# Kernel optimization log

Hardware: AMD Instinct MI355X
Metric: run time of the kernel (lower is better)

Reference implementation:

```python
import jax, jax.numpy as jnp
import numpy as np

N = 64          # num_atoms
K = 2           # num_edge_types
VDIM = 32
EDIM = 32
HID = 64        # hard-coded n_hid in the module
B = 128         # num_sims
E = N * (N - 1)
_off = ~np.eye(N, dtype=bool)
SEND, RECV = [np.asarray(a) for a in np.where(_off)]  # edge e: node SEND[e] -> node RECV[e] (NRI: rel_send=rows, rel_rec=cols)
EPS = 1e-5  # torch BatchNorm1d default


def _mlp(x, W1, b1, W2, b2, gamma, beta):
    # NRI MLP: fc1 -> ELU -> fc2 -> ELU -> BatchNorm1d (training-mode batch stats over all but last dim)
    h = jax.nn.elu(x @ W1 + b1)
    o = jax.nn.elu(h @ W2 + b2)
    ax = tuple(range(o.ndim - 1))
    mu = o.mean(ax, keepdims=True)
    var = o.var(ax, keepdims=True)  # biased variance, as torch BN uses for normalization
    return gamma * (o - mu) * jax.lax.rsqrt(var + EPS) + beta


def setup_inputs():
    key = jax.random.key(0)
    ks = jax.random.split(key, 16)
    p = lambda k, shape: jax.random.normal(k, shape, jnp.float32) * 0.05
    return {
        "v0": jax.random.normal(ks[0], (B, N, VDIM), jnp.float32),
        "e0": jax.random.normal(ks[1], (B, N, N - 1, EDIM), jnp.float32),
        "edge_type": jax.random.uniform(ks[2], (B, E, K), dtype=jnp.float32),
        "mlpv_W1": p(ks[3], (EDIM, HID)), "mlpv_b1": p(ks[4], (HID,)),
        "mlpv_W2": p(ks[5], (HID, VDIM)), "mlpv_b2": p(ks[6], (VDIM,)),
        "mlpv_gamma": jnp.ones((VDIM,), jnp.float32), "mlpv_beta": jnp.zeros((VDIM,), jnp.float32),
        "mlpe_W1": p(ks[7], (K, 2 * VDIM, HID)), "mlpe_b1": p(ks[8], (K, HID)),
        "mlpe_W2": p(ks[9], (K, HID, EDIM)), "mlpe_b2": p(ks[10], (K, EDIM)),
        "mlpe_gamma": jnp.ones((K, EDIM), jnp.float32), "mlpe_beta": jnp.zeros((K, EDIM), jnp.float32),
    }


def reference(v0, e0, edge_type, mlpv_W1, mlpv_b1, mlpv_W2, mlpv_b2, mlpv_gamma, mlpv_beta,
              mlpe_W1, mlpe_b1, mlpe_W2, mlpe_b2, mlpe_gamma, mlpe_beta):
    e0f = e0.reshape(B, E, EDIM)
    # edge2node: rel_rec.T @ e0f is exactly a scatter-add of edge states onto receiver nodes, / num_atoms
    agg = jnp.zeros((B, N, EDIM), e0f.dtype).at[:, RECV].add(e0f) / N
    dv = _mlp(agg, mlpv_W1, mlpv_b1, mlpv_W2, mlpv_b2, mlpv_gamma, mlpv_beta)  # [B,N,VDIM]
    # node2edge: rel_rec@v0 / rel_send@v0 are gathers of node states per edge
    edges = jnp.concatenate([v0[:, RECV], v0[:, SEND]], axis=-1)  # [B,E,2V]
    # all K per-edge-type MLPs in one batched einsum (replaces the Python loop)
    h = jax.nn.elu(jnp.einsum('bef,kfh->bkeh', edges, mlpe_W1) + mlpe_b1[None, :, None, :])
    o = jax.nn.elu(jnp.einsum('bkeh,kho->bkeo', h, mlpe_W2) + mlpe_b2[None, :, None, :])
    mu = o.mean((0, 2), keepdims=True)   # BN stats per edge type, over (batch, edges)
    var = o.var((0, 2), keepdims=True)
    o = mlpe_gamma[None, :, None, :] * (o - mu) * jax.lax.rsqrt(var + EPS) + mlpe_beta[None, :, None, :]
    # mask each type's message by its edge_type weight, then sum over types
    de = (o * edge_type.transpose(0, 2, 1)[..., None]).sum(1)  # [B,E,EDIM]
    de = de.reshape(B, N, N - 1, EDIM)
    return (dv, de, edge_type * 0)
```

## Files before the change

### kernel.cpp

```cpp
#include <hip/hip_runtime.h>
#include <hip/hip_bf16.h>

#define NB 128
#define NA 64
#define NE 4032
#define KT 2
#define BE (NB * NE)
#define DV_SIZE 262144
#define DE_SIZE 16515072
#define ZERO_SIZE 1032192

#define PBLK_A 1008
#define TPW_A 8

typedef __attribute__((ext_vector_type(8))) short short8;
typedef __attribute__((ext_vector_type(4))) float floatx4;

__device__ __forceinline__ float elu(float x) {
    return x > 0.0f ? x : __expf(x) - 1.0f;
}

__device__ __forceinline__ unsigned short f2bf(float x) {
    unsigned u = __float_as_uint(x);
    return (unsigned short)((u + 0x7FFFu + ((u >> 16) & 1u)) >> 16);
}

__device__ __forceinline__ unsigned pkbf(float a, float b) {
    __hip_bfloat162 h = __float22bfloat162_rn(make_float2(a, b));
    unsigned u;
    __builtin_memcpy(&u, &h, 4);
    return u;
}

__device__ __forceinline__ short8 pack8(float4 a, float4 b) {
    unsigned u[4] = {pkbf(a.x, a.y), pkbf(a.z, a.w), pkbf(b.x, b.y), pkbf(b.z, b.w)};
    short8 r;
    __builtin_memcpy(&r, u, 16);
    return r;
}

__global__ __launch_bounds__(256) void cvt_v0_kernel(const float* __restrict__ v0,
                                                     unsigned short* __restrict__ v0bf) {
    const int idx = blockIdx.x * 256 + threadIdx.x;
    const float4 v = reinterpret_cast<const float4*>(v0)[idx];
    uint2 r;
    r.x = pkbf(v.x, v.y);
    r.y = pkbf(v.z, v.w);
    reinterpret_cast<uint2*>(v0bf)[idx] = r;
}

struct SMW {
    short8 wA1[16][64];
    short8 wA2[8][64];
    float b1s[128];
    float b2s[64];
};

__device__ __forceinline__ void stage_weights(SMW& sm, const float* __restrict__ W1,
                                              const float* __restrict__ b1,
                                              const float* __restrict__ W2,
                                              const float* __restrict__ b2) {
    const int tid = threadIdx.x;
#pragma unroll
    for (int s = 0; s < 4; s++) {
        const int slot = s * 256 + tid;
        const int f = slot >> 6, l = slot & 63;
        const int k = f >> 3, mt = (f >> 1) & 3, kf = f & 1;
        const int g = l >> 4, m15 = l & 15;
        short8 v;
#pragma unroll
        for (int j = 0; j < 8; j++) {
            const int kk = kf * 32 + g * 8 + j;
            v[j] = (short)f2bf(W1[(k * 64 + kk) * 64 + mt * 16 + m15]);
        }
        sm.wA1[f][l] = v;
    }
#pragma unroll
    for (int s = 0; s < 2; s++) {
        const int slot = s * 256 + tid;
        const int f = slot >> 6, l = slot & 63;
        const int k = f >> 2, mt2 = (f >> 1) & 1, kf = f & 1;
        const int g = l >> 4, m15 = l & 15;
        short8 v;
#pragma unroll
        for (int j = 0; j < 8; j++) {
            const int kk = kf * 32 + g * 8 + j;
            v[j] = (short)f2bf(W2[(k * 64 + kk) * 32 + mt2 * 16 + m15]);
        }
        sm.wA2[f][l] = v;
    }
    if (tid < 128) sm.b1s[tid] = b1[tid];
    if (tid < 64) sm.b2s[tid] = b2[tid];
}

__device__ __forceinline__ void load_xfrags(const unsigned short* __restrict__ v0bf,
                                            int row, int g, short8& bx0, short8& bx1) {
    const int b = row / NE;
    const int e = row - b * NE;
    const int i = e / 63;
    const int p = e - i * 63;
    const int j = p + (p >= i ? 1 : 0);
    bx0 = *(const short8*)(v0bf + ((b * 64 + j) * 32 + g * 8));
    bx1 = *(const short8*)(v0bf + ((b * 64 + i) * 32 + g * 8));
}

__global__ __launch_bounds__(256, 3) void edge_stats_mfma_kernel(
    const unsigned short* __restrict__ v0bf, const float* __restrict__ W1,
    const float* __restrict__ b1, const float* __restrict__ W2,
    const float* __restrict__ b2, float* __restrict__ buckets,
    unsigned short* __restrict__ o_e) {
    __shared__ SMW sm;
    __shared__ unsigned hbuf[4][512];
    stage_weights(sm, W1, b1, W2, b2);
    __syncthreads();

    const int lane = threadIdx.x & 63;
    const int w = threadIdx.x >> 6;
    const int g = lane >> 4, m15 = lane & 15;
    const int gw = blockIdx.x * 4 + w;
    unsigned* hw = &hbuf[w][0];
    const int sw = m15 & 7;
    const int rbase = m15 * 32;

#pragma unroll 1
    for (int k = 0; k < 2; k++) {
        short8 a1r[4][2], a2r[2][2];
#pragma unroll
        for (int mt = 0; mt < 4; mt++)
#pragma unroll
            for (int kf = 0; kf < 2; kf++)
                a1r[mt][kf] = sm.wA1[(k * 4 + mt) * 2 + kf][lane];
#pragma unroll
        for (int mt2 = 0; mt2 < 2; mt2++)
#pragma unroll
            for (int kf = 0; kf < 2; kf++)
                a2r[mt2][kf] = sm.wA2[(k * 2 + mt2) * 2 + kf][lane];

        float st[2][4], sq[2][4];
#pragma unroll
        for (int m = 0; m < 2; m++)
#pragma unroll
            for (int r = 0; r < 4; r++) { st[m][r] = 0.f; sq[m][r] = 0.f; }

#pragma unroll 1
        for (int tt = 0; tt < TPW_A; tt++) {
            const int row = (gw * TPW_A + tt) * 16 + m15;
            short8 bx0, bx1;
            load_xfrags(v0bf, row, g, bx0, bx1);

#pragma unroll
            for (int mt = 0; mt < 4; mt++) {
                const float4 bb = *(const float4*)&sm.b1s[k * 64 + mt * 16 + 4 * g];
                floatx4 acc = {bb.x, bb.y, bb.z, bb.w};
                acc = __builtin_amdgcn_mfma_f32_16x16x32_bf16(a1r[mt][0], bx0, acc, 0, 0, 0);
                acc = __builtin_amdgcn_mfma_f32_16x16x32_bf16(a1r[mt][1], bx1, acc, 0, 0, 0);
                uint2 hv;
                hv.x = pkbf(elu(acc[0]), elu(acc[1]));
                hv.y = pkbf(elu(acc[2]), elu(acc[3]));
                const int q = 2 * mt + (g >> 1);
                *(uint2*)&hw[rbase + ((q ^ sw) << 2) + 2 * (g & 1)] = hv;
            }
            const short8 bh0 = *(const short8*)&hw[rbase + (((g) ^ sw) << 2)];
            const short8 bh1 = *(const short8*)&hw[rbase + (((g + 4) ^ sw) << 2)];
#pragma unroll
            for (int mt2 = 0; mt2 < 2; mt2++) {
                const float4 bb = *(const float4*)&sm.b2s[k * 32 + mt2 * 16 + 4 * g];
                floatx4 acc = {bb.x, bb.y, bb.z, bb.w};
                acc = __builtin_amdgcn_mfma_f32_16x16x32_bf16(a2r[mt2][0], bh0, acc, 0, 0, 0);
                acc = __builtin_amdgcn_mfma_f32_16x16x32_bf16(a2r[mt2][1], bh1, acc, 0, 0, 0);
                float v0v = elu(acc[0]), v1v = elu(acc[1]);
                float v2v = elu(acc[2]), v3v = elu(acc[3]);
                st[mt2][0] += v0v; sq[mt2][0] += v0v * v0v;
                st[mt2][1] += v1v; sq[mt2][1] += v1v * v1v;
                st[mt2][2] += v2v; sq[mt2][2] += v2v * v2v;
                st[mt2][3] += v3v; sq[mt2][3] += v3v * v3v;
                uint2 ov;
                ov.x = pkbf(v0v, v1v);
                ov.y = pkbf(v2v, v3v);
                *(uint2*)(o_e + ((size_t)k * BE + row) * 32 + mt2 * 16 + 4 * g) = ov;
            }
        }

        const int bk = gw & 31;
#pragma unroll
        for (int m = 0; m < 2; m++)
#pragma unroll
            for (int r = 0; r < 4; r++) {
                float s = st[m][r], ss = sq[m][r];
#pragma unroll
                for (int off = 1; off < 16; off <<= 1) {
                    s += __shfl_xor(s, off, 64);
                    ss += __shfl_xor(ss, off, 64);
                }
                if (m15 == 0) {
                    const int ch = m * 16 + 4 * g + r;
                    atomicAdd(&buckets[((bk * KT + k) * 32 + ch) * 2], s);
                    atomicAdd(&buckets[((bk * KT + k) * 32 + ch) * 2 + 1], ss);
                }
            }
    }
}

__global__ void edge_stats_final_kernel(const float* __restrict__ buckets,
                                        const float* __restrict__ gamma,
                                        const float* __restrict__ beta,
                                        float* __restrict__ statf) {
    const int t = threadIdx.x;
    if (t >= 64) return;
    const int k = t >> 5, c = t & 31;
    float s = 0.0f, ss = 0.0f;
#pragma unroll 1
    for (int bk = 0; bk < 32; bk++) {
        s += buckets[((bk * KT + k) * 32 + c) * 2];
        ss += buckets[((bk * KT + k) * 32 + c) * 2 + 1];
    }
    const float M = (float)BE;
    const float mu = s / M;
    const float var = ss / M - mu * mu;
    const float rs = rsqrtf(var + 1e-5f);
    const float af = gamma[k * 32 + c] * rs;
    statf[t * 2] = af;
    statf[t * 2 + 1] = beta[k * 32 + c] - mu * af;
}

__global__ __launch_bounds__(256) void edge_epilogue_kernel(
    const unsigned short* __restrict__ o_e, const float* __restrict__ etype,
    const float* __restrict__ statf, float* __restrict__ de) {
    __shared__ float afs[64], cfs[64];
    if (threadIdx.x < 64) {
        afs[threadIdx.x] = statf[threadIdx.x * 2];
        cfs[threadIdx.x] = statf[threadIdx.x * 2 + 1];
    }
    __syncthreads();

    const int t = blockIdx.x * 256 + threadIdx.x;
    const int cg = t & 3;
    const int row = t >> 2;
    const uint4 p0 = *(const uint4*)(o_e + (size_t)row * 32 + cg * 8);
    const uint4 p1 = *(const uint4*)(o_e + ((size_t)BE + row) * 32 + cg * 8);
    const float2 wv = *(const float2*)(etype + (size_t)row * 2);
    const unsigned pu0[4] = {p0.x, p0.y, p0.z, p0.w};
    const unsigned pu1[4] = {p1.x, p1.y, p1.z, p1.w};

    float r[8];
#pragma unroll
    for (int u = 0; u < 8; u++) {
        const int ch = cg * 8 + u;
        const float o0 = __uint_as_float((u & 1) ? (pu0[u >> 1] & 0xFFFF0000u)
                                                 : (pu0[u >> 1] << 16));
        const float o1 = __uint_as_float((u & 1) ? (pu1[u >> 1] & 0xFFFF0000u)
                                                 : (pu1[u >> 1] << 16));
        r[u] = wv.x * fmaf(afs[ch], o0, cfs[ch]) +
               wv.y * fmaf(afs[32 + ch], o1, cfs[32 + ch]);
    }
    float4* dst = (float4*)(de + (size_t)row * 32 + cg * 8);
    dst[0] = make_float4(r[0], r[1], r[2], r[3]);
    dst[1] = make_float4(r[4], r[5], r[6], r[7]);
}

__global__ __launch_bounds__(256) void agg_kernel(const float* __restrict__ e0,
                                                  float* __restrict__ agg) {
    const int f = blockIdx.x * 256 + threadIdx.x;
    const int c4 = f & 7;
    const int jn = (f >> 3) & 63;
    const int b = f >> 9;
    const float4* base = (const float4*)e0 + (size_t)b * 64 * 63 * 8;
    float x = 0.f, y = 0.f, z = 0.f, ww = 0.f;
#pragma unroll 4
    for (int i = 0; i < 64; i++) {
        int p = jn - (jn > i ? 1 : 0);
        p = p > 62 ? 62 : p;
        const float m = (i == jn) ? 0.0f : 1.0f;
        const float4 v = base[(i * 63 + p) * 8 + c4];
        x = fmaf(v.x, m, x);
        y = fmaf(v.y, m, y);
        z = fmaf(v.z, m, z);
        ww = fmaf(v.w, m, ww);
    }
    const float s = 1.0f / 64.0f;
    *(float4*)(agg + (size_t)f * 4) = make_float4(x * s, y * s, z * s, ww * s);
}

struct SMN {
    short8 wA1n[4][64];
    short8 wA2n[4][64];
    float b1s[64];
    float b2s[32];
    unsigned long long hbuf[4][16 * 20];
};

__global__ __launch_bounds__(256) void node_mlp_mfma_kernel(
    const float* __restrict__ agg, const float* __restrict__ W1,
    const float* __restrict__ b1, const float* __restrict__ W2,
    const float* __restrict__ b2, float* __restrict__ o_v,
    float* __restrict__ nbuckets) {
    __shared__ SMN sm;
    const int tid = threadIdx.x;
    {
        const int f = tid >> 6, l = tid & 63;
        const int g = l >> 4, m15 = l & 15;
        short8 v;
#pragma unroll
        for (int j = 0; j < 8; j++)
            v[j] = (short)f2bf(W1[(g * 8 + j) * 64 + f * 16 + m15]);
        sm.wA1n[f][l] = v;
        const int mt2 = f >> 1, kf = f & 1;
        short8 u;
#pragma unroll
        for (int j = 0; j < 8; j++)
            u[j] = (short)f2bf(W2[(kf * 32 + g * 8 + j) * 32 + mt2 * 16 + m15]);
        sm.wA2n[f][l] = u;
    }
    if (tid < 64) sm.b1s[tid] = b1[tid];
    else if (tid < 96) sm.b2s[tid - 64] = b2[tid - 64];
    __syncthreads();

    const int lane = tid & 63;
    const int w = tid >> 6;
    const int g = lane >> 4, m15 = lane & 15;
    const int tile = blockIdx.x * 4 + w;
    const int row = tile * 16 + m15;

    const float4* px = (const float4*)(agg + (size_t)row * 32 + g * 8);
    const short8 bx = pack8(px[0], px[1]);

    const char* hbase = (const char*)&sm.hbuf[w][0];
    unsigned long long* hw = &sm.hbuf[w][0];

#pragma unroll
    for (int mt = 0; mt < 4; mt++) {
        const float4 bb = *(const float4*)&sm.b1s[mt * 16 + 4 * g];
        floatx4 acc = {bb.x, bb.y, bb.z, bb.w};
        acc = __builtin_amdgcn_mfma_f32_16x16x32_bf16(sm.wA1n[mt][lane], bx, acc, 0, 0, 0);
        const unsigned lo = pkbf(elu(acc[0]), elu(acc[1]));
        const unsigned hi = pkbf(elu(acc[2]), elu(acc[3]));
        hw[m15 * 20 + mt * 4 + g] = ((unsigned long long)hi << 32) | lo;
    }
    const short8 bh0 = *(const short8*)(hbase + m15 * 160 + 0 + g * 16);
    const short8 bh1 = *(const short8*)(hbase + m15 * 160 + 64 + g * 16);

    const int bk = tile & 31;
#pragma unroll
    for (int mt2 = 0; mt2 < 2; mt2++) {
        const float4 bb = *(const float4*)&sm.b2s[mt2 * 16 + 4 * g];
        floatx4 acc = {bb.x, bb.y, bb.z, bb.w};
        acc = __builtin_amdgcn_mfma_f32_16x16x32_bf16(sm.wA2n[mt2 * 2 + 0][lane], bh0, acc, 0, 0, 0);
        acc = __builtin_amdgcn_mfma_f32_16x16x32_bf16(sm.wA2n[mt2 * 2 + 1][lane], bh1, acc, 0, 0, 0);
        float4 ov;
        ov.x = elu(acc[0]);
        ov.y = elu(acc[1]);
        ov.z = elu(acc[2]);
        ov.w = elu(acc[3]);
        *(float4*)(o_v + (size_t)row * 32 + mt2 * 16 + 4 * g) = ov;
        const float vv[4] = {ov.x, ov.y, ov.z, ov.w};
#pragma unroll
        for (int r = 0; r < 4; r++) {
            float s = vv[r], ss = vv[r] * vv[r];
#pragma unroll
            for (int off = 1; off < 16; off <<= 1) {
                s += __shfl_xor(s, off, 64);
                ss += __shfl_xor(ss, off, 64);
            }
            if (m15 == 0) {
                const int ch = mt2 * 16 + 4 * g + r;
                atomicAdd(&nbuckets[(bk * 32 + ch) * 2], s);
                atomicAdd(&nbuckets[(bk * 32 + ch) * 2 + 1], ss);
            }
        }
    }
}

__global__ void node_stats_final_kernel(const float* __restrict__ nbuckets,
                                        const float* __restrict__ gamma,
                                        const float* __restrict__ beta,
                                        float* __restrict__ statn) {
    const int c = threadIdx.x;
    if (c >= 32) return;
    float s = 0.0f, ss = 0.0f;
#pragma unroll 1
    for (int bk = 0; bk < 32; bk++) {
        s += nbuckets[(bk * 32 + c) * 2];
        ss += nbuckets[(bk * 32 + c) * 2 + 1];
    }
    const float M = 8192.0f;
    const float mu = s / M;
    const float var = ss / M - mu * mu;
    const float rs = rsqrtf(var + 1e-5f);
    const float af = gamma[c] * rs;
    statn[c * 2] = af;
    statn[c * 2 + 1] = beta[c] - mu * af;
}

__global__ __launch_bounds__(256) void node_norm_kernel(
    const float* __restrict__ o_v, const float* __restrict__ statn,
    float* __restrict__ dv) {
    const int f = blockIdx.x * 256 + threadIdx.x;
    const int c = f & 31;
    dv[f] = statn[c * 2] * o_v[f] + statn[c * 2 + 1];
}

extern "C" void kernel_launch(void* const* d_in, const int* in_sizes, int n_in,
                              void* d_out, int out_size, void* d_ws, size_t ws_size,
                              hipStream_t stream) {
    const float* v0 = (const float*)d_in[0];
    const float* e0 = (const float*)d_in[1];
    const float* etype = (const float*)d_in[2];
    const float* W1v = (const float*)d_in[3];
    const float* b1v = (const float*)d_in[4];
    const float* W2v = (const float*)d_in[5];
    const float* b2v = (const float*)d_in[6];
    const float* gv = (const float*)d_in[7];
    const float* btv = (const float*)d_in[8];
    const float* W1e = (const float*)d_in[9];
    const float* b1e = (const float*)d_in[10];
    const float* W2e = (const float*)d_in[11];
    const float* b2e = (const float*)d_in[12];
    const float* ge = (const float*)d_in[13];
    const float* bte = (const float*)d_in[14];
    float* out = (float*)d_out;

    float* ws = (float*)d_ws;
    float* buckets = ws;
    float* statf = ws + 4096;
    float* nbuckets = ws + 4224;
    float* statn = ws + 6272;
    float* agg = ws + 6336;
    float* o_v = ws + 268480;
    unsigned short* v0bf = (unsigned short*)(ws + 530624);
    unsigned short* o_e = (unsigned short*)(ws + 661696);

    hipMemsetAsync(buckets, 0, (4096 + 128 + 2048) * sizeof(float), stream);
    hipMemsetAsync(out + DV_SIZE + DE_SIZE, 0, ZERO_SIZE * sizeof(float), stream);

    cvt_v0_kernel<<<256, 256, 0, stream>>>(v0, v0bf);
    agg_kernel<<<256, 256, 0, stream>>>(e0, agg);
    node_mlp_mfma_kernel<<<128, 256, 0, stream>>>(agg, W1v, b1v, W2v, b2v, o_v, nbuckets);
    node_stats_final_kernel<<<1, 64, 0, stream>>>(nbuckets, gv, btv, statn);
    node_norm_kernel<<<1024, 256, 0, stream>>>(o_v, statn, out);
    edge_stats_mfma_kernel<<<PBLK_A, 256, 0, stream>>>(v0bf, W1e, b1e, W2e, b2e,
                                                       buckets, o_e);
    edge_stats_final_kernel<<<1, 64, 0, stream>>>(buckets, ge, bte, statf);
    edge_epilogue_kernel<<<8064, 256, 0, stream>>>(o_e, etype, statf, out + DV_SIZE);
}
```

Before: 261.2 us.

## Merge small kernels, fold BN stat finalization into epilogue, halve edge LDS

Fuses the v0 bf16 conversion with the edge aggregation into one prep kernel. It folds both BatchNorm stat-finalization kernels into a single combined edge/node epilogue, where each block recomputes the stats redundantly. The edge MLP kernel now stages only one edge type's weights at a time, which halves shared memory. That lets it raise the occupancy hint and double the grid with fewer tiles per wave. The aim is to cut launch count and raise occupancy, at the cost of redundant bucket reads in every epilogue block and more stat atomics.

```diff
diff --git a/kernel.cpp b/kernel.cpp
--- a/kernel.cpp
+++ b/kernel.cpp
@@ -10,8 +10,11 @@
 #define DE_SIZE 16515072
 #define ZERO_SIZE 1032192
 
-#define PBLK_A 1008
-#define TPW_A 8
+#define PBLK_A 2016
+#define TPW_A 4
+
+#define EPI_EDGE_BLOCKS 8064
+#define EPI_NODE_BLOCKS 1024
 
 typedef __attribute__((ext_vector_type(8))) short short8;
 typedef __attribute__((ext_vector_type(4))) float floatx4;
@@ -39,58 +42,84 @@
     return r;
 }
 
-__global__ __launch_bounds__(256) void cvt_v0_kernel(const float* __restrict__ v0,
-                                                     unsigned short* __restrict__ v0bf) {
-    const int idx = blockIdx.x * 256 + threadIdx.x;
-    const float4 v = reinterpret_cast<const float4*>(v0)[idx];
-    uint2 r;
-    r.x = pkbf(v.x, v.y);
-    r.y = pkbf(v.z, v.w);
-    reinterpret_cast<uint2*>(v0bf)[idx] = r;
-}
-
-struct SMW {
-    short8 wA1[16][64];
-    short8 wA2[8][64];
-    float b1s[128];
-    float b2s[64];
+__global__ __launch_bounds__(256) void prep_kernel(const float* __restrict__ e0,
+                                                   float* __restrict__ agg,
+                                                   const float* __restrict__ v0,
+                                                   unsigned short* __restrict__ v0bf) {
+    if (blockIdx.x < 256) {
+        const int f = blockIdx.x * 256 + threadIdx.x;
+        const int c4 = f & 7;
+        const int jn = (f >> 3) & 63;
+        const int b = f >> 9;
+        const float4* base = (const float4*)e0 + (size_t)b * 64 * 63 * 8;
+        float x = 0.f, y = 0.f, z = 0.f, ww = 0.f;
+#pragma unroll 8
+        for (int i = 0; i < 64; i++) {
+            int p = jn - (jn > i ? 1 : 0);
+            p = p > 62 ? 62 : p;
+            const float m = (i == jn) ? 0.0f : 1.0f;
+            const float4 v = base[(i * 63 + p) * 8 + c4];
+            x = fmaf(v.x, m, x);
+            y = fmaf(v.y, m, y);
+            z = fmaf(v.z, m, z);
+            ww = fmaf(v.w, m, ww);
+        }
+        const float s = 1.0f / 64.0f;
+        *(float4*)(agg + (size_t)f * 4) = make_float4(x * s, y * s, z * s, ww * s);
+    } else {
+        const int idx = (blockIdx.x - 256) * 256 + threadIdx.x;
+        const float4 v = reinterpret_cast<const float4*>(v0)[idx];
+        uint2 r;
+        r.x = pkbf(v.x, v.y);
+        r.y = pkbf(v.z, v.w);
+        reinterpret_cast<uint2*>(v0bf)[idx] = r;
+    }
+}
+
+struct SMWk {
+    short8 wA1[8][64];
+    short8 wA2[4][64];
+    float b1s[64];
+    float b2s[32];
 };
-
-__device__ __forceinline__ void stage_weights(SMW& sm, const float* __restrict__ W1,
-                                              const float* __restrict__ b1,
-                                              const float* __restrict__ W2,
-                                              const float* __restrict__ b2) {
+struct SME {
+    SMWk wk;
+    unsigned hbuf[4][512];
+};
+
+__device__ __forceinline__ void stage_weights_k(SMWk& sm, const float* __restrict__ W1,
+                                                const float* __restrict__ b1,
+                                                const float* __restrict__ W2,
+                                                const float* __restrict__ b2) {
     const int tid = threadIdx.x;
-#pragma unroll
-    for (int s = 0; s < 4; s++) {
-        const int slot = s * 256 + tid;
-        const int f = slot >> 6, l = slot & 63;
-        const int k = f >> 3, mt = (f >> 1) & 3, kf = f & 1;
-        const int g = l >> 4, m15 = l & 15;
-        short8 v;
-#pragma unroll
-        for (int j = 0; j < 8; j++) {
-            const int kk = kf * 32 + g * 8 + j;
-            v[j] = (short)f2bf(W1[(k * 64 + kk) * 64 + mt * 16 + m15]);
-        }
-        sm.wA1[f][l] = v;
-    }
 #pragma unroll
     for (int s = 0; s < 2; s++) {
         const int slot = s * 256 + tid;
         const int f = slot >> 6, l = slot & 63;
-        const int k = f >> 2, mt2 = (f >> 1) & 1, kf = f & 1;
+        const int mt = f >> 1, kf = f & 1;
         const int g = l >> 4, m15 = l & 15;
         short8 v;
 #pragma unroll
         for (int j = 0; j < 8; j++) {
             const int kk = kf * 32 + g * 8 + j;
-            v[j] = (short)f2bf(W2[(k * 64 + kk) * 32 + mt2 * 16 + m15]);
+            v[j] = (short)f2bf(W1[kk * 64 + mt * 16 + m15]);
+        }
+        sm.wA1[f][l] = v;
+    }
+    {
+        const int f = tid >> 6, l = tid & 63;
+        const int mt2 = f >> 1, kf = f & 1;
+        const int g = l >> 4, m15 = l & 15;
+        short8 v;
+#pragma unroll
+        for (int j = 0; j < 8; j++) {
+            const int kk = kf * 32 + g * 8 + j;
+            v[j] = (short)f2bf(W2[kk * 32 + mt2 * 16 + m15]);
         }
         sm.wA2[f][l] = v;
     }
-    if (tid < 128) sm.b1s[tid] = b1[tid];
-    if (tid < 64) sm.b2s[tid] = b2[tid];
+    if (tid < 64) sm.b1s[tid] = b1[tid];
+    else if (tid < 96) sm.b2s[tid - 64] = b2[tid - 64];
 }
 
 __device__ __forceinline__ void load_xfrags(const unsigned short* __restrict__ v0bf,
@@ -104,37 +133,37 @@
     bx1 = *(const short8*)(v0bf + ((b * 64 + i) * 32 + g * 8));
 }
 
-__global__ __launch_bounds__(256, 3) void edge_stats_mfma_kernel(
+__global__ __launch_bounds__(256, 6) void edge_stats_mfma_kernel(
     const unsigned short* __restrict__ v0bf, const float* __restrict__ W1,
     const float* __restrict__ b1, const float* __restrict__ W2,
     const float* __restrict__ b2, float* __restrict__ buckets,
     unsigned short* __restrict__ o_e) {
-    __shared__ SMW sm;
-    __shared__ unsigned hbuf[4][512];
-    stage_weights(sm, W1, b1, W2, b2);
-    __syncthreads();
-
+    __shared__ SME sm;
     const int lane = threadIdx.x & 63;
     const int w = threadIdx.x >> 6;
     const int g = lane >> 4, m15 = lane & 15;
     const int gw = blockIdx.x * 4 + w;
-    unsigned* hw = &hbuf[w][0];
+    unsigned* hw = &sm.hbuf[w][0];
     const int sw = m15 & 7;
     const int rbase = m15 * 32;
 
 #pragma unroll 1
     for (int k = 0; k < 2; k++) {
+        if (k) __syncthreads();
+        stage_weights_k(sm.wk, W1 + k * 4096, b1 + k * 64, W2 + k * 2048, b2 + k * 32);
+        __syncthreads();
+
         short8 a1r[4][2], a2r[2][2];
 #pragma unroll
         for (int mt = 0; mt < 4; mt++)
 #pragma unroll
             for (int kf = 0; kf < 2; kf++)
-                a1r[mt][kf] = sm.wA1[(k * 4 + mt) * 2 + kf][lane];
+                a1r[mt][kf] = sm.wk.wA1[mt * 2 + kf][lane];
 #pragma unroll
         for (int mt2 = 0; mt2 < 2; mt2++)
 #pragma unroll
             for (int kf = 0; kf < 2; kf++)
-                a2r[mt2][kf] = sm.wA2[(k * 2 + mt2) * 2 + kf][lane];
+                a2r[mt2][kf] = sm.wk.wA2[mt2 * 2 + kf][lane];
 
         float st[2][4], sq[2][4];
 #pragma unroll
@@ -150,7 +179,7 @@
 
 #pragma unroll
             for (int mt = 0; mt < 4; mt++) {
-                const float4 bb = *(const float4*)&sm.b1s[k * 64 + mt * 16 + 4 * g];
+                const float4 bb = *(const float4*)&sm.wk.b1s[mt * 16 + 4 * g];
                 floatx4 acc = {bb.x, bb.y, bb.z, bb.w};
                 acc = __builtin_amdgcn_mfma_f32_16x16x32_bf16(a1r[mt][0], bx0, acc, 0, 0, 0);
                 acc = __builtin_amdgcn_mfma_f32_16x16x32_bf16(a1r[mt][1], bx1, acc, 0, 0, 0);
@@ -162,9 +191,10 @@
             }
             const short8 bh0 = *(const short8*)&hw[rbase + (((g) ^ sw) << 2)];
             const short8 bh1 = *(const short8*)&hw[rbase + (((g + 4) ^ sw) << 2)];
+            unsigned short* op = o_e + ((size_t)k * BE + row) * 32 + 4 * g;
 #pragma unroll
             for (int mt2 = 0; mt2 < 2; mt2++) {
-                const float4 bb = *(const float4*)&sm.b2s[k * 32 + mt2 * 16 + 4 * g];
+                const float4 bb = *(const float4*)&sm.wk.b2s[mt2 * 16 + 4 * g];
                 floatx4 acc = {bb.x, bb.y, bb.z, bb.w};
                 acc = __builtin_amdgcn_mfma_f32_16x16x32_bf16(a2r[mt2][0], bh0, acc, 0, 0, 0);
                 acc = __builtin_amdgcn_mfma_f32_16x16x32_bf16(a2r[mt2][1], bh1, acc, 0, 0, 0);
@@ -177,7 +207,7 @@
                 uint2 ov;
                 ov.x = pkbf(v0v, v1v);
                 ov.y = pkbf(v2v, v3v);
-                *(uint2*)(o_e + ((size_t)k * BE + row) * 32 + mt2 * 16 + 4 * g) = ov;
+                *(uint2*)(op + mt2 * 16) = ov;
             }
         }
 
@@ -199,86 +229,6 @@
                 }
             }
     }
-}
-
-__global__ void edge_stats_final_kernel(const float* __restrict__ buckets,
-                                        const float* __restrict__ gamma,
-                                        const float* __restrict__ beta,
-                                        float* __restrict__ statf) {
-    const int t = threadIdx.x;
-    if (t >= 64) return;
-    const int k = t >> 5, c = t & 31;
-    float s = 0.0f, ss = 0.0f;
-#pragma unroll 1
-    for (int bk = 0; bk < 32; bk++) {
-        s += buckets[((bk * KT + k) * 32 + c) * 2];
-        ss += buckets[((bk * KT + k) * 32 + c) * 2 + 1];
-    }
-    const float M = (float)BE;
-    const float mu = s / M;
-    const float var = ss / M - mu * mu;
-    const float rs = rsqrtf(var + 1e-5f);
-    const float af = gamma[k * 32 + c] * rs;
-    statf[t * 2] = af;
-    statf[t * 2 + 1] = beta[k * 32 + c] - mu * af;
-}
-
-__global__ __launch_bounds__(256) void edge_epilogue_kernel(
-    const unsigned short* __restrict__ o_e, const float* __restrict__ etype,
-    const float* __restrict__ statf, float* __restrict__ de) {
-    __shared__ float afs[64], cfs[64];
-    if (threadIdx.x < 64) {
-        afs[threadIdx.x] = statf[threadIdx.x * 2];
-        cfs[threadIdx.x] = statf[threadIdx.x * 2 + 1];
-    }
-    __syncthreads();
-
-    const int t = blockIdx.x * 256 + threadIdx.x;
-    const int cg = t & 3;
-    const int row = t >> 2;
-    const uint4 p0 = *(const uint4*)(o_e + (size_t)row * 32 + cg * 8);
-    const uint4 p1 = *(const uint4*)(o_e + ((size_t)BE + row) * 32 + cg * 8);
-    const float2 wv = *(const float2*)(etype + (size_t)row * 2);
-    const unsigned pu0[4] = {p0.x, p0.y, p0.z, p0.w};
-    const unsigned pu1[4] = {p1.x, p1.y, p1.z, p1.w};
-
-    float r[8];
-#pragma unroll
-    for (int u = 0; u < 8; u++) {
-        const int ch = cg * 8 + u;
-        const float o0 = __uint_as_float((u & 1) ? (pu0[u >> 1] & 0xFFFF0000u)
-                                                 : (pu0[u >> 1] << 16));
-        const float o1 = __uint_as_float((u & 1) ? (pu1[u >> 1] & 0xFFFF0000u)
-                                                 : (pu1[u >> 1] << 16));
-        r[u] = wv.x * fmaf(afs[ch], o0, cfs[ch]) +
-               wv.y * fmaf(afs[32 + ch], o1, cfs[32 + ch]);
-    }
-    float4* dst = (float4*)(de + (size_t)row * 32 + cg * 8);
-    dst[0] = make_float4(r[0], r[1], r[2], r[3]);
-    dst[1] = make_float4(r[4], r[5], r[6], r[7]);
-}
-
-__global__ __launch_bounds__(256) void agg_kernel(const float* __restrict__ e0,
-                                                  float* __restrict__ agg) {
-    const int f = blockIdx.x * 256 + threadIdx.x;
-    const int c4 = f & 7;
-    const int jn = (f >> 3) & 63;
-    const int b = f >> 9;
-    const float4* base = (const float4*)e0 + (size_t)b * 64 * 63 * 8;
-    float x = 0.f, y = 0.f, z = 0.f, ww = 0.f;
-#pragma unroll 4
-    for (int i = 0; i < 64; i++) {
-        int p = jn - (jn > i ? 1 : 0);
-        p = p > 62 ? 62 : p;
-        const float m = (i == jn) ? 0.0f : 1.0f;
-        const float4 v = base[(i * 63 + p) * 8 + c4];
-        x = fmaf(v.x, m, x);
-        y = fmaf(v.y, m, y);
-        z = fmaf(v.z, m, z);
-        ww = fmaf(v.w, m, ww);
-    }
-    const float s = 1.0f / 64.0f;
-    *(float4*)(agg + (size_t)f * 4) = make_float4(x * s, y * s, z * s, ww * s);
 }
 
 struct SMN {
@@ -370,33 +320,79 @@
     }
 }
 
-__global__ void node_stats_final_kernel(const float* __restrict__ nbuckets,
-                                        const float* __restrict__ gamma,
-                                        const float* __restrict__ beta,
-                                        float* __restrict__ statn) {
-    const int c = threadIdx.x;
-    if (c >= 32) return;
-    float s = 0.0f, ss = 0.0f;
-#pragma unroll 1
-    for (int bk = 0; bk < 32; bk++) {
-        s += nbuckets[(bk * 32 + c) * 2];
-        ss += nbuckets[(bk * 32 + c) * 2 + 1];
-    }
-    const float M = 8192.0f;
-    const float mu = s / M;
-    const float var = ss / M - mu * mu;
-    const float rs = rsqrtf(var + 1e-5f);
-    const float af = gamma[c] * rs;
-    statn[c * 2] = af;
-    statn[c * 2 + 1] = beta[c] - mu * af;
-}
-
-__global__ __launch_bounds__(256) void node_norm_kernel(
-    const float* __restrict__ o_v, const float* __restrict__ statn,
-    float* __restrict__ dv) {
-    const int f = blockIdx.x * 256 + threadIdx.x;
-    const int c = f & 31;
-    dv[f] = statn[c * 2] * o_v[f] + statn[c * 2 + 1];
+__global__ __launch_bounds__(256) void epilogue_kernel(
+    const unsigned short* __restrict__ o_e, const float* __restrict__ etype,
+    const float* __restrict__ buckets, const float* __restrict__ ge,
+    const float* __restrict__ bte, const float* __restrict__ o_v,
+    const float* __restrict__ nbuckets, const float* __restrict__ gv,
+    const float* __restrict__ btv, float* __restrict__ out) {
+    __shared__ float afs[64], cfs[64];
+
+    if (blockIdx.x < EPI_EDGE_BLOCKS) {
+        if (threadIdx.x < 64) {
+            const int k = threadIdx.x >> 5, c = threadIdx.x & 31;
+            float s = 0.0f, ss = 0.0f;
+#pragma unroll
+            for (int bk = 0; bk < 32; bk++) {
+                s += buckets[((bk * KT + k) * 32 + c) * 2];
+                ss += buckets[((bk * KT + k) * 32 + c) * 2 + 1];
+            }
+            const float M = (float)BE;
+            const float mu = s / M;
+            const float var = ss / M - mu * mu;
+            const float rs = rsqrtf(var + 1e-5f);
+            const float af = ge[k * 32 + c] * rs;
+            afs[threadIdx.x] = af;
+            cfs[threadIdx.x] = bte[k * 32 + c] - mu * af;
+        }
+        __syncthreads();
+
+        float* de = out + DV_SIZE;
+        const int t = blockIdx.x * 256 + threadIdx.x;
+        const int cg = t & 3;
+        const int row = t >> 2;
+        const uint4 p0 = *(const uint4*)(o_e + (size_t)row * 32 + cg * 8);
+        const uint4 p1 = *(const uint4*)(o_e + ((size_t)BE + row) * 32 + cg * 8);
+        const float2 wv = *(const float2*)(etype + (size_t)row * 2);
+        const unsigned pu0[4] = {p0.x, p0.y, p0.z, p0.w};
+        const unsigned pu1[4] = {p1.x, p1.y, p1.z, p1.w};
+
+        float r[8];
+#pragma unroll
+        for (int u = 0; u < 8; u++) {
+            const int ch = cg * 8 + u;
+            const float o0 = __uint_as_float((u & 1) ? (pu0[u >> 1] & 0xFFFF0000u)
+                                                     : (pu0[u >> 1] << 16));
+            const float o1 = __uint_as_float((u & 1) ? (pu1[u >> 1] & 0xFFFF0000u)
+                                                     : (pu1[u >> 1] << 16));
+            r[u] = wv.x * fmaf(afs[ch], o0, cfs[ch]) +
+                   wv.y * fmaf(afs[32 + ch], o1, cfs[32 + ch]);
+        }
+        float4* dst = (float4*)(de + (size_t)row * 32 + cg * 8);
+        dst[0] = make_float4(r[0], r[1], r[2], r[3]);
+        dst[1] = make_float4(r[4], r[5], r[6], r[7]);
+    } else {
+        if (threadIdx.x < 32) {
+            const int c = threadIdx.x;
+            float s = 0.0f, ss = 0.0f;
+#pragma unroll
+            for (int bk = 0; bk < 32; bk++) {
+                s += nbuckets[(bk * 32 + c) * 2];
+                ss += nbuckets[(bk * 32 + c) * 2 + 1];
+            }
+            const float M = 8192.0f;
+            const float mu = s / M;
+            const float var = ss / M - mu * mu;
+            const float rs = rsqrtf(var + 1e-5f);
+            const float af = gv[c] * rs;
+            afs[c] = af;
+            cfs[c] = btv[c] - mu * af;
+        }
+        __syncthreads();
+        const int f = (blockIdx.x - EPI_EDGE_BLOCKS) * 256 + threadIdx.x;
+        const int c = f & 31;
+        out[f] = afs[c] * o_v[f] + cfs[c];
+    }
 }
 
 extern "C" void kernel_launch(void* const* d_in, const int* in_sizes, int n_in,
@@ -421,24 +417,19 @@
 
     float* ws = (float*)d_ws;
     float* buckets = ws;
-    float* statf = ws + 4096;
-    float* nbuckets = ws + 4224;
-    float* statn = ws + 6272;
-    float* agg = ws + 6336;
-    float* o_v = ws + 268480;
-    unsigned short* v0bf = (unsigned short*)(ws + 530624);
-    unsigned short* o_e = (unsigned short*)(ws + 661696);
-
-    hipMemsetAsync(buckets, 0, (4096 + 128 + 2048) * sizeof(float), stream);
+    float* nbuckets = ws + 4096;
+    float* agg = ws + 6144;
+    float* o_v = ws + 268288;
+    unsigned short* v0bf = (unsigned short*)(ws + 530432);
+    unsigned short* o_e = (unsigned short*)(ws + 661504);
+
+    hipMemsetAsync(buckets, 0, (4096 + 2048) * sizeof(float), stream);
     hipMemsetAsync(out + DV_SIZE + DE_SIZE, 0, ZERO_SIZE * sizeof(float), stream);
 
-    cvt_v0_kernel<<<256, 256, 0, stream>>>(v0, v0bf);
-    agg_kernel<<<256, 256, 0, stream>>>(e0, agg);
+    prep_kernel<<<512, 256, 0, stream>>>(e0, agg, v0, v0bf);
     node_mlp_mfma_kernel<<<128, 256, 0, stream>>>(agg, W1v, b1v, W2v, b2v, o_v, nbuckets);
-    node_stats_final_kernel<<<1, 64, 0, stream>>>(nbuckets, gv, btv, statn);
-    node_norm_kernel<<<1024, 256, 0, stream>>>(o_v, statn, out);
     edge_stats_mfma_kernel<<<PBLK_A, 256, 0, stream>>>(v0bf, W1e, b1e, W2e, b2e,
                                                        buckets, o_e);
-    edge_stats_final_kernel<<<1, 64, 0, stream>>>(buckets, ge, bte, statf);
-    edge_epilogue_kernel<<<8064, 256, 0, stream>>>(o_e, etype, statf, out + DV_SIZE);
-}
+    epilogue_kernel<<<EPI_EDGE_BLOCKS + EPI_NODE_BLOCKS, 256, 0, stream>>>(
+        o_e, etype, buckets, ge, bte, o_v, nbuckets, gv, btv, out);
+}
```

Result: slower. 369.4 us (+41.5%).
